# Optimization experiments

Measured on AMD Instinct MI355X. Metric: run time of the kernel, lower is better.

## Reference

```python
import jax, jax.numpy as jnp
import numpy as np

EPS = 0.5
MIN_SAMPLES = 5


def setup_inputs() -> dict:
    key = jax.random.key(0)
    X = jax.random.uniform(key, (12288, 8), dtype=jnp.float32)
    return {"X": X}


def reference(X):
    """DBSCAN: eps-range queries + cluster expansion, expressed as
    eps-graph connected components over core points (same clustering
    as the serial BFS in the original module; cluster ids are assigned
    in order of each cluster's minimum core index, matching the
    ascending-scan discovery order of the original)."""
    N = X.shape[0]
    SENTINEL = jnp.int32(N)

    # pairwise squared Euclidean distances [N, N] (KDTree range query equivalent)
    sq = jnp.sum(X * X, axis=1)
    d2 = sq[:, None] + sq[None, :] - 2.0 * (X @ X.T)
    adj = d2 <= (EPS * EPS)                      # eps-neighborhood (includes self)

    density = jnp.sum(adj, axis=1)               # |query_ball_point(x_i, eps)|
    core = density >= MIN_SAMPLES                # core-point mask

    # core-core edges: BFS expansion only propagates through cores
    core_adj = adj & core[None, :] & core[:, None]

    idx = jnp.arange(N, dtype=jnp.int32)
    init = jnp.where(core, idx, SENTINEL)        # each core starts as its own root

    def prop(lbl):
        # min label over core neighbors (min-plus propagation = connected components)
        nb_min = jnp.min(jnp.where(core_adj, lbl[None, :], SENTINEL), axis=1)
        return jnp.minimum(lbl, nb_min)

    def cond(state):
        cur, prev = state
        return jnp.any(cur != prev)

    def body(state):
        cur, _ = state
        return prop(cur), cur

    lbl, _ = jax.lax.while_loop(cond, body, (prop(init), init))

    # border points: non-core points within eps of a core join that core's cluster
    core_nb = jnp.min(jnp.where(adj & core[None, :], lbl[None, :], SENTINEL), axis=1)
    root = jnp.where(core, lbl, core_nb)         # SENTINEL -> noise

    # compact cluster ids: rank of each cluster root (min core index) ascending,
    # matching the original's sequential discovery order k = 0, 1, ...
    is_root = core & (lbl == idx)
    rank = jnp.cumsum(is_root.astype(jnp.int32)) - 1   # rank[i] valid where is_root[i]
    labels = jnp.where(root < SENTINEL,
                       rank[jnp.clip(root, 0, N - 1)],
                       jnp.int32(-1))
    return labels
```

## Files before the change

kernel.cpp:

```cpp
#include <hip/hip_runtime.h>

#define NPTS 12288
#define DIMS 8
#define EPS2 0.25f
#define MINS 5
#define NIB1 (NPTS / 256)
#define NW   (NPTS / 32)
#define SENT NPTS
#define RMAX 512
#define W    (RMAX / 32)
#define BIGL 0x3fffffff
#define FT   128
#define FB   256
#define FBGRID 256

#define ATHR 256
#define AROWS 2
#define ATI  (ATHR * AROWS)
#define ANIB (NPTS / ATI)
#define ANJB 48
#define AJC  (NPTS / ANJB)
#define AWCH (AJC / 32)

typedef float v2f __attribute__((ext_vector_type(2)));

__device__ __forceinline__ float dot8(const v2f* xi, const float4& a, const float4& b) {
  v2f y0 = {a.x, a.y}, y1 = {a.z, a.w}, y2 = {b.x, b.y}, y3 = {b.z, b.w};
  v2f d = xi[0] * y0;
  d = __builtin_elementwise_fma(xi[1], y1, d);
  d = __builtin_elementwise_fma(xi[2], y2, d);
  d = __builtin_elementwise_fma(xi[3], y3, d);
  return d.x + d.y;
}


__global__ __launch_bounds__(ATHR) void k_adj(const float* __restrict__ X,
                                              unsigned int* __restrict__ adj,
                                              int* __restrict__ density) {
  __shared__ float4 xs[AJC][2];
  __shared__ float sqs[AJC];
  int t = threadIdx.x;
  int j0 = blockIdx.y * AJC;
  {
    int j = j0 + t;
    float4 a = ((const float4*)X)[j * 2];
    float4 b = ((const float4*)X)[j * 2 + 1];
    xs[t][0] = a; xs[t][1] = b;
    float sv = 0.f;
    sv = fmaf(a.x, a.x, sv); sv = fmaf(a.y, a.y, sv); sv = fmaf(a.z, a.z, sv); sv = fmaf(a.w, a.w, sv);
    sv = fmaf(b.x, b.x, sv); sv = fmaf(b.y, b.y, sv); sv = fmaf(b.z, b.z, sv); sv = fmaf(b.w, b.w, sv);
    sqs[t] = sv;
  }
  int i0 = blockIdx.x * ATI + t, i1 = i0 + ATHR;
  v2f xi0[4], xi1[4];
  {
    float4 a0 = ((const float4*)X)[i0 * 2], b0v = ((const float4*)X)[i0 * 2 + 1];
    float4 a1 = ((const float4*)X)[i1 * 2], b1v = ((const float4*)X)[i1 * 2 + 1];
    xi0[0] = (v2f){a0.x, a0.y}; xi0[1] = (v2f){a0.z, a0.w};
    xi0[2] = (v2f){b0v.x, b0v.y}; xi0[3] = (v2f){b0v.z, b0v.w};
    xi1[0] = (v2f){a1.x, a1.y}; xi1[1] = (v2f){a1.z, a1.w};
    xi1[2] = (v2f){b1v.x, b1v.y}; xi1[3] = (v2f){b1v.z, b1v.w};
  }
  float sq0 = 0.f, sq1 = 0.f;
#pragma unroll
  for (int q = 0; q < 4; q++) {
    v2f p0 = xi0[q] * xi0[q], p1 = xi1[q] * xi1[q];
    sq0 += p0.x + p0.y; sq1 += p1.x + p1.y;
  }
  __syncthreads();
  unsigned int acc0[AWCH], acc1[AWCH];
#pragma unroll
  for (int w = 0; w < AWCH; w++) {
    unsigned int b0 = 0u, b1 = 0u;
#pragma unroll 4
    for (int bit = 0; bit < 32; bit++) {
      int jj = (w << 5) + bit;
      float4 xa = xs[jj][0], xb = xs[jj][1];
      float sj = sqs[jj];
      unsigned int m = 1u << bit;
      float d20 = (sq0 + sj) - 2.0f * dot8(xi0, xa, xb);
      float d21 = (sq1 + sj) - 2.0f * dot8(xi1, xa, xb);
      if (d20 <= EPS2) b0 |= m;
      if (d21 <= EPS2) b1 |= m;
    }
    acc0[w] = b0; acc1[w] = b1;
  }
  uint4* dst0 = (uint4*)(adj + (size_t)i0 * NW + blockIdx.y * AWCH);
  uint4* dst1 = (uint4*)(adj + (size_t)i1 * NW + blockIdx.y * AWCH);
  dst0[0] = make_uint4(acc0[0], acc0[1], acc0[2], acc0[3]);
  dst0[1] = make_uint4(acc0[4], acc0[5], acc0[6], acc0[7]);
  dst1[0] = make_uint4(acc1[0], acc1[1], acc1[2], acc1[3]);
  dst1[1] = make_uint4(acc1[4], acc1[5], acc1[6], acc1[7]);
  int pc0 = 0, pc1 = 0;
#pragma unroll
  for (int w = 0; w < AWCH; w++) { pc0 += __popc(acc0[w]); pc1 += __popc(acc1[w]); }
  atomicAdd(&density[i0], pc0);
  atomicAdd(&density[i1], pc1);
}

__global__ __launch_bounds__(256) void k_core(const int* __restrict__ density,
                                              unsigned long long* __restrict__ corebm,
                                              unsigned int* __restrict__ bm) {
  int t = threadIdx.x;
  if (blockIdx.x == 0) {
#pragma unroll
    for (int q = 0; q < RMAX * W / 256; q++) bm[t + q * 256] = 0u;
  }
  int i = blockIdx.x * 256 + t;
  unsigned long long m = __ballot(density[i] >= MINS);
  if ((t & 63) == 0) corebm[i >> 6] = m;
}

__global__ __launch_bounds__(256) void k_hookbm(const unsigned int* __restrict__ adj,
                                                const unsigned int* __restrict__ cb32,
                                                int* __restrict__ hook) {
  __shared__ unsigned int cb[NW];
  int t = threadIdx.x;
  for (int w = t; w < NW; w += 256) cb[w] = cb32[w];
  __syncthreads();
  int i = blockIdx.x * 256 + t;
  const unsigned int* row = adj + (size_t)i * NW;
  int wi = i >> 5;
  int m = i;
  for (int w = 0; w <= wi; w++) {
    unsigned int x = row[w] & cb[w];
    if (w == wi) x &= (1u << (i & 31)) - 1;
    if (x) { m = (w << 5) + __ffs(x) - 1; break; }
  }
  hook[i] = m;
}

__global__ __launch_bounds__(1024) void k_rid(const int* __restrict__ density,
                                              const int* __restrict__ hook,
                                              int* __restrict__ Rptr,
                                              int* __restrict__ labL,
                                              int* __restrict__ bcount) {
  __shared__ unsigned short ridS[NPTS];
  __shared__ int wsum[16];
  int t = threadIdx.x;
  int lane = t & 63, wid = t >> 6;
  const int SEG = NPTS / 1024;
  int base = t * SEG;
  int flags = 0;
  int s = 0;
#pragma unroll
  for (int k = 0; k < SEG; k++) {
    int i = base + k;
    int f = (density[i] >= MINS && hook[i] == i) ? 1 : 0;
    flags |= f << k;
    s += f;
  }
  int segsum = s;
#pragma unroll
  for (int off = 1; off < 64; off <<= 1) {
    int n = __shfl_up(s, off, 64);
    if (lane >= off) s += n;
  }
  if (lane == 63) wsum[wid] = s;
  __syncthreads();
  int woff = 0;
  for (int w = 0; w < wid; w++) woff += wsum[w];
  int run = woff + s - segsum;
#pragma unroll
  for (int k = 0; k < SEG; k++) {
    ridS[base + k] = (unsigned short)run;
    run += (flags >> k) & 1;
  }
  if (t == 1023) *Rptr = run;
  if (t == 0) *bcount = 0;
  __syncthreads();
  for (int k = 0; k < SEG; k++) {
    int i = base + k;
    int lab = -1;
    if (density[i] >= MINS) {
      int v = i, h = hook[v];
      while (h != v) { v = h; h = hook[v]; }
      lab = min((int)ridS[v], RMAX - 1);
    }
    labL[i] = lab;
  }
}

__global__ __launch_bounds__(FB) void k_fillbm(const unsigned int* __restrict__ adj,
                                               const unsigned int* __restrict__ cb32,
                                               const int* __restrict__ labL,
                                               unsigned int* __restrict__ bm) {
  __shared__ unsigned int bmL[RMAX * W];
  __shared__ unsigned short labS[NPTS];
  __shared__ unsigned int cb[NW];
  int t = threadIdx.x;
  for (int q = t; q < RMAX * W; q += FB) bmL[q] = 0u;
  for (int q = t; q < NPTS; q += FB) labS[q] = (unsigned short)(labL[q] + 1);
  for (int w = t; w < NW; w += FB) cb[w] = cb32[w];
  __syncthreads();
  int lane = t & 63, wv = t >> 6;
  int gw = blockIdx.x * 4 + wv;
  for (int i = gw; i < NPTS; i += 4 * FBGRID) {
    int a0 = (int)labS[i] - 1;
    if (a0 < 0) continue;
    const unsigned int* row = adj + (size_t)i * NW;
    int wi = i >> 5;
    for (int w = wi + lane; w < NW; w += 64) {
      unsigned int x = row[w] & cb[w];
      if (w == wi) x &= (0xFFFFFFFEu << (i & 31));
      while (x) {
        int b = __ffs(x) - 1; x &= x - 1;
        int lj = (int)labS[(w << 5) + b] - 1;
        if (lj != a0) {
          atomicOr(&bmL[a0 * W + (lj >> 5)], 1u << (lj & 31));
          atomicOr(&bmL[lj * W + (a0 >> 5)], 1u << (a0 & 31));
        }
      }
    }
  }
  __syncthreads();
  for (int q = t; q < RMAX * W; q += FB) {
    unsigned int v = bmL[q];
    if (v) atomicOr(&bm[q], v);
  }
}

__global__ __launch_bounds__(RMAX) void k_cc(const unsigned int* __restrict__ bm,
                                             const int* __restrict__ Rptr,
                                             int* __restrict__ clab) {
  __shared__ int lbl[RMAX];
  __shared__ int mn[RMAX];
  __shared__ int chg, cmp;
  int a = threadIdx.x;
  int R = *Rptr; if (R > RMAX) R = RMAX;
  lbl[a] = a;
  __syncthreads();
  while (true) {
    int m = lbl[a];
    if (a < R) {
      const unsigned int* row = bm + a * W;
#pragma unroll
      for (int w = 0; w < W; w++) {
        unsigned int bits = row[w];
        while (bits) {
          int b = __ffs(bits) - 1;
          bits &= bits - 1;
          m = min(m, lbl[(w << 5) + b]);
        }
      }
    }
    mn[a] = m;
    if (a == 0) chg = 0;
    __syncthreads();
    int l = lbl[a];
    if (m < l) { atomicMin(&lbl[l], m); atomicMin(&lbl[a], m); chg = 1; }
    __syncthreads();
    while (true) {
      if (a == 0) cmp = 0;
      __syncthreads();
      int nl = lbl[lbl[a]];
      __syncthreads();
      if (nl < lbl[a]) { lbl[a] = nl; cmp = 1; }
      __syncthreads();
      if (!cmp) break;
    }
    if (!chg) break;
    __syncthreads();
  }
  int flag = (a < R && lbl[a] == a) ? 1 : 0;
  mn[a] = flag;
  __syncthreads();
  for (int off = 1; off < RMAX; off <<= 1) {
    int v = mn[a];
    int add = (a >= off) ? mn[a - off] : 0;
    __syncthreads();
    mn[a] = v + add;
    __syncthreads();
  }
  clab[a] = mn[lbl[a]] - 1;
}

__global__ __launch_bounds__(256) void k_labels(const int* __restrict__ labL,
                                                const int* __restrict__ clab,
                                                int* __restrict__ labArr,
                                                int* __restrict__ blist,
                                                int* __restrict__ bcount,
                                                float* __restrict__ out) {
  int i = blockIdx.x * blockDim.x + threadIdx.x;
  if (i >= NPTS) return;
  int a = labL[i];
  if (a >= 0) {
    int lab = clab[a];
    labArr[i] = lab;
    out[i] = (float)lab;
  } else {
    labArr[i] = BIGL;
    out[i] = -1.0f;
    int pos = atomicAdd(bcount, 1);
    blist[pos] = i;
  }
}

__global__ __launch_bounds__(FT) void k_border(const unsigned int* __restrict__ adj,
                                               const unsigned int* __restrict__ cb32,
                                               const int* __restrict__ labArr,
                                               const int* __restrict__ blist,
                                               const int* __restrict__ bcount,
                                               float* __restrict__ out) {
  __shared__ unsigned int cb[NW];
  __shared__ int wm[FT / 64];
  int t = threadIdx.x;
  for (int w = t; w < NW; w += FT) cb[w] = cb32[w];
  __syncthreads();
  int count = *bcount;
  for (int k = blockIdx.x; k < count; k += gridDim.x) {
    int p = blist[k];
    const unsigned int* row = adj + (size_t)p * NW;
    int m = BIGL;
    for (int w = t; w < NW; w += FT) {
      unsigned int x = row[w] & cb[w];
      while (x) {
        int b = __ffs(x) - 1; x &= x - 1;
        m = min(m, labArr[(w << 5) + b]);
      }
    }
#pragma unroll
    for (int off = 32; off >= 1; off >>= 1) m = min(m, __shfl_xor(m, off, 64));
    if ((t & 63) == 0) wm[t >> 6] = m;
    __syncthreads();
    if (t == 0) {
      int mm = min(wm[0], wm[1]);
      out[p] = (mm < BIGL) ? (float)mm : -1.0f;
    }
    __syncthreads();
  }
}


extern "C" void kernel_launch(void* const* d_in, const int* in_sizes, int n_in,
                              void* d_out, int out_size, void* d_ws, size_t ws_size,
                              hipStream_t stream) {
  const float* X = (const float*)d_in[0];
  float* out = (float*)d_out;

  char* ws = (char*)d_ws;
  unsigned int* adj = (unsigned int*)ws;
  size_t off = (size_t)NPTS * NW * 4;
  int* density = (int*)(ws + off);           off += 4 * NPTS;
  int* hook    = (int*)(ws + off);           off += 4 * NPTS;
  int* labL    = (int*)(ws + off);           off += 4 * NPTS;
  int* labArr  = (int*)(ws + off);           off += 4 * NPTS;
  int* blist   = (int*)(ws + off);           off += 4 * NPTS;
  unsigned long long* corebm = (unsigned long long*)(ws + off); off += 2048;
  unsigned int* bm  = (unsigned int*)(ws + off); off += 4 * RMAX * W;
  int* clab    = (int*)(ws + off);           off += 4 * RMAX;
  int* Rptr    = (int*)(ws + off);
  int* bcount  = Rptr + 1;

  hipMemsetAsync(density, 0, 4 * NPTS, stream);

  dim3 gridA(ANIB, ANJB);

  k_adj<<<gridA, ATHR, 0, stream>>>(X, adj, density);
  k_core<<<NIB1, 256, 0, stream>>>(density, corebm, bm);
  k_hookbm<<<NIB1, 256, 0, stream>>>(adj, (const unsigned int*)corebm, hook);
  k_rid<<<1, 1024, 0, stream>>>(density, hook, Rptr, labL, bcount);
  k_fillbm<<<FBGRID, FB, 0, stream>>>(adj, (const unsigned int*)corebm, labL, bm);
  k_cc<<<1, RMAX, 0, stream>>>(bm, Rptr, clab);
  k_labels<<<NIB1, 256, 0, stream>>>(labL, clab, labArr, blist, bcount, out);
  k_border<<<256, FT, 0, stream>>>(adj, (const unsigned int*)corebm, labArr, blist, bcount, out);
}
```

Before: 229.1 us.

## Restructure adjacency kernel to build bitmask words via wavefront ballots

The adjacency kernel now assigns j-points to lanes and loops over a shared-memory tile of i-points. Each comparison becomes a wavefront ballot that directly yields a 64-bit mask, replacing per-thread serial bit assembly. Masks are transposed through double-buffered shared memory so each row is written with coalesced uint4 stores. Density is accumulated per j-column, which relies on the adjacency being symmetric; this adds a block barrier per 64-row group and extra select instructions per comparison.

```diff
diff --git a/kernel.cpp b/kernel.cpp
--- a/kernel.cpp
+++ b/kernel.cpp
@@ -14,88 +14,99 @@
 #define FB   256
 #define FBGRID 256
 
-#define ATHR 256
-#define AROWS 2
-#define ATI  (ATHR * AROWS)
-#define ANIB (NPTS / ATI)
-#define ANJB 48
-#define AJC  (NPTS / ANJB)
-#define AWCH (AJC / 32)
+#define AIT 256
+#define AJT 512
 
 typedef float v2f __attribute__((ext_vector_type(2)));
 
-__device__ __forceinline__ float dot8(const v2f* xi, const float4& a, const float4& b) {
-  v2f y0 = {a.x, a.y}, y1 = {a.z, a.w}, y2 = {b.x, b.y}, y3 = {b.z, b.w};
-  v2f d = xi[0] * y0;
-  d = __builtin_elementwise_fma(xi[1], y1, d);
-  d = __builtin_elementwise_fma(xi[2], y2, d);
-  d = __builtin_elementwise_fma(xi[3], y3, d);
-  return d.x + d.y;
-}
-
-
-__global__ __launch_bounds__(ATHR) void k_adj(const float* __restrict__ X,
-                                              unsigned int* __restrict__ adj,
-                                              int* __restrict__ density) {
-  __shared__ float4 xs[AJC][2];
-  __shared__ float sqs[AJC];
-  int t = threadIdx.x;
-  int j0 = blockIdx.y * AJC;
+__device__ __forceinline__ float sq8(const float4& a, const float4& b) {
+  float sv = 0.f;
+  sv = fmaf(a.x, a.x, sv); sv = fmaf(a.y, a.y, sv);
+  sv = fmaf(a.z, a.z, sv); sv = fmaf(a.w, a.w, sv);
+  sv = fmaf(b.x, b.x, sv); sv = fmaf(b.y, b.y, sv);
+  sv = fmaf(b.z, b.z, sv); sv = fmaf(b.w, b.w, sv);
+  return sv;
+}
+
+
+__global__ __launch_bounds__(256) void k_adj(const float* __restrict__ X,
+                                             unsigned int* __restrict__ adj,
+                                             int* __restrict__ density) {
+  __shared__ float4 xsh[AIT][2];
+  __shared__ float sqsh[AIT];
+  __shared__ uint4 tr[2][4][64];
+  const int t = threadIdx.x;
+  const int w = t >> 6, lane = t & 63;
+  const int i0 = blockIdx.x * AIT;
+  const int j0 = blockIdx.y * AJT;
+
   {
-    int j = j0 + t;
-    float4 a = ((const float4*)X)[j * 2];
-    float4 b = ((const float4*)X)[j * 2 + 1];
-    xs[t][0] = a; xs[t][1] = b;
-    float sv = 0.f;
-    sv = fmaf(a.x, a.x, sv); sv = fmaf(a.y, a.y, sv); sv = fmaf(a.z, a.z, sv); sv = fmaf(a.w, a.w, sv);
-    sv = fmaf(b.x, b.x, sv); sv = fmaf(b.y, b.y, sv); sv = fmaf(b.z, b.z, sv); sv = fmaf(b.w, b.w, sv);
-    sqs[t] = sv;
-  }
-  int i0 = blockIdx.x * ATI + t, i1 = i0 + ATHR;
-  v2f xi0[4], xi1[4];
+    float4 a = ((const float4*)X)[(size_t)(i0 + t) * 2];
+    float4 b = ((const float4*)X)[(size_t)(i0 + t) * 2 + 1];
+    xsh[t][0] = a; xsh[t][1] = b;
+    sqsh[t] = sq8(a, b);
+  }
+
+  const int ja = j0 + w * 128 + lane;
+  const int jb = ja + 64;
+  v2f xja[4], xjb[4];
+  float sqja, sqjb;
   {
-    float4 a0 = ((const float4*)X)[i0 * 2], b0v = ((const float4*)X)[i0 * 2 + 1];
-    float4 a1 = ((const float4*)X)[i1 * 2], b1v = ((const float4*)X)[i1 * 2 + 1];
-    xi0[0] = (v2f){a0.x, a0.y}; xi0[1] = (v2f){a0.z, a0.w};
-    xi0[2] = (v2f){b0v.x, b0v.y}; xi0[3] = (v2f){b0v.z, b0v.w};
-    xi1[0] = (v2f){a1.x, a1.y}; xi1[1] = (v2f){a1.z, a1.w};
-    xi1[2] = (v2f){b1v.x, b1v.y}; xi1[3] = (v2f){b1v.z, b1v.w};
-  }
-  float sq0 = 0.f, sq1 = 0.f;
-#pragma unroll
-  for (int q = 0; q < 4; q++) {
-    v2f p0 = xi0[q] * xi0[q], p1 = xi1[q] * xi1[q];
-    sq0 += p0.x + p0.y; sq1 += p1.x + p1.y;
-  }
-  __syncthreads();
-  unsigned int acc0[AWCH], acc1[AWCH];
-#pragma unroll
-  for (int w = 0; w < AWCH; w++) {
-    unsigned int b0 = 0u, b1 = 0u;
-#pragma unroll 4
-    for (int bit = 0; bit < 32; bit++) {
-      int jj = (w << 5) + bit;
-      float4 xa = xs[jj][0], xb = xs[jj][1];
-      float sj = sqs[jj];
-      unsigned int m = 1u << bit;
-      float d20 = (sq0 + sj) - 2.0f * dot8(xi0, xa, xb);
-      float d21 = (sq1 + sj) - 2.0f * dot8(xi1, xa, xb);
-      if (d20 <= EPS2) b0 |= m;
-      if (d21 <= EPS2) b1 |= m;
-    }
-    acc0[w] = b0; acc1[w] = b1;
-  }
-  uint4* dst0 = (uint4*)(adj + (size_t)i0 * NW + blockIdx.y * AWCH);
-  uint4* dst1 = (uint4*)(adj + (size_t)i1 * NW + blockIdx.y * AWCH);
-  dst0[0] = make_uint4(acc0[0], acc0[1], acc0[2], acc0[3]);
-  dst0[1] = make_uint4(acc0[4], acc0[5], acc0[6], acc0[7]);
-  dst1[0] = make_uint4(acc1[0], acc1[1], acc1[2], acc1[3]);
-  dst1[1] = make_uint4(acc1[4], acc1[5], acc1[6], acc1[7]);
-  int pc0 = 0, pc1 = 0;
-#pragma unroll
-  for (int w = 0; w < AWCH; w++) { pc0 += __popc(acc0[w]); pc1 += __popc(acc1[w]); }
-  atomicAdd(&density[i0], pc0);
-  atomicAdd(&density[i1], pc1);
+    float4 a = ((const float4*)X)[(size_t)ja * 2];
+    float4 b = ((const float4*)X)[(size_t)ja * 2 + 1];
+    xja[0] = (v2f){a.x, a.y}; xja[1] = (v2f){a.z, a.w};
+    xja[2] = (v2f){b.x, b.y}; xja[3] = (v2f){b.z, b.w};
+    sqja = sq8(a, b);
+  }
+  {
+    float4 a = ((const float4*)X)[(size_t)jb * 2];
+    float4 b = ((const float4*)X)[(size_t)jb * 2 + 1];
+    xjb[0] = (v2f){a.x, a.y}; xjb[1] = (v2f){a.z, a.w};
+    xjb[2] = (v2f){b.x, b.y}; xjb[3] = (v2f){b.z, b.w};
+    sqjb = sq8(a, b);
+  }
+
+  int dj0 = 0, dj1 = 0;
+  __syncthreads();
+
+  for (int g = 0; g < AIT / 64; ++g) {
+    unsigned int r0 = 0, r1 = 0, r2 = 0, r3 = 0;
+#pragma unroll 16
+    for (int ii = 0; ii < 64; ++ii) {
+      int i = (g << 6) + ii;
+      float4 A = xsh[i][0], B = xsh[i][1];
+      float si = sqsh[i];
+      v2f d0 = (v2f){A.x, A.y} * xja[0];
+      d0 = __builtin_elementwise_fma((v2f){A.z, A.w}, xja[1], d0);
+      d0 = __builtin_elementwise_fma((v2f){B.x, B.y}, xja[2], d0);
+      d0 = __builtin_elementwise_fma((v2f){B.z, B.w}, xja[3], d0);
+      v2f d1 = (v2f){A.x, A.y} * xjb[0];
+      d1 = __builtin_elementwise_fma((v2f){A.z, A.w}, xjb[1], d1);
+      d1 = __builtin_elementwise_fma((v2f){B.x, B.y}, xjb[2], d1);
+      d1 = __builtin_elementwise_fma((v2f){B.z, B.w}, xjb[3], d1);
+      float d20 = (si + sqja) - 2.0f * (d0.x + d0.y);
+      float d21 = (si + sqjb) - 2.0f * (d1.x + d1.y);
+      bool c0 = d20 <= EPS2;
+      bool c1 = d21 <= EPS2;
+      unsigned long long m0 = __ballot(c0);
+      unsigned long long m1 = __ballot(c1);
+      dj0 += c0; dj1 += c1;
+      unsigned int m0lo = (unsigned int)m0, m0hi = (unsigned int)(m0 >> 32);
+      unsigned int m1lo = (unsigned int)m1, m1hi = (unsigned int)(m1 >> 32);
+      bool mine = (lane == ii);
+      r0 = mine ? m0lo : r0;
+      r1 = mine ? m0hi : r1;
+      r2 = mine ? m1lo : r2;
+      r3 = mine ? m1hi : r3;
+    }
+    tr[g & 1][w][lane] = make_uint4(r0, r1, r2, r3);
+    __syncthreads();
+    uint4 v = tr[g & 1][t & 3][t >> 2];
+    *(uint4*)(adj + (size_t)(i0 + (g << 6) + (t >> 2)) * NW
+              + blockIdx.y * 16 + (t & 3) * 4) = v;
+  }
+  atomicAdd(&density[ja], dj0);
+  atomicAdd(&density[jb], dj1);
 }
 
 __global__ __launch_bounds__(256) void k_core(const int* __restrict__ density,
@@ -354,9 +365,9 @@
 
   hipMemsetAsync(density, 0, 4 * NPTS, stream);
 
-  dim3 gridA(ANIB, ANJB);
-
-  k_adj<<<gridA, ATHR, 0, stream>>>(X, adj, density);
+  dim3 gridA(NPTS / AIT, NPTS / AJT);
+
+  k_adj<<<gridA, 256, 0, stream>>>(X, adj, density);
   k_core<<<NIB1, 256, 0, stream>>>(density, corebm, bm);
   k_hookbm<<<NIB1, 256, 0, stream>>>(adj, (const unsigned int*)corebm, hook);
   k_rid<<<1, 1024, 0, stream>>>(density, hook, Rptr, labL, bcount);
```

Result: slower. 240.4 us (+4.9%).

## Exploit adjacency symmetry: compute upper-triangular tiles and mirror via bit transpose

Applied to the files above, without the earlier changes.

The pairwise-distance bitmask kernel now launches only the upper-triangular tile blocks (600 instead of 24x48) and writes each tile both directly and transposed. The transpose uses a 32x32 bit transpose via warp shuffles plus a shared-memory staging buffer. Diagonal tiles use masked partial writes so that no entry is written twice. This roughly halves the distance arithmetic, but adds shuffles, shared-memory traffic, a barrier and an extra set of scattered global stores and atomics per block.

```diff
diff --git a/kernel.cpp b/kernel.cpp
--- a/kernel.cpp
+++ b/kernel.cpp
@@ -17,10 +17,9 @@
 #define ATHR 256
 #define AROWS 2
 #define ATI  (ATHR * AROWS)
-#define ANIB (NPTS / ATI)
-#define ANJB 48
-#define AJC  (NPTS / ANJB)
+#define AJC  256
 #define AWCH (AJC / 32)
+#define NBLK 600
 
 typedef float v2f __attribute__((ext_vector_type(2)));
 
@@ -33,16 +32,38 @@
   return d.x + d.y;
 }
 
+__device__ __forceinline__ unsigned int tr32(unsigned int x, int lane31) {
+  const unsigned int M[5] = {0x0000FFFFu, 0x00FF00FFu, 0x0F0F0F0Fu,
+                             0x33333333u, 0x55555555u};
+  const int S[5] = {16, 8, 4, 2, 1};
+#pragma unroll
+  for (int k = 0; k < 5; ++k) {
+    int s = S[k];
+    unsigned int m = M[k];
+    unsigned int p = __shfl_xor(x, s, 32);
+    x = (lane31 & s) ? ((x & ~m) | ((p >> s) & m))
+                     : ((x & m) | ((p & m) << s));
+  }
+  return x;
+}
+
 
 __global__ __launch_bounds__(ATHR) void k_adj(const float* __restrict__ X,
                                               unsigned int* __restrict__ adj,
                                               int* __restrict__ density) {
   __shared__ float4 xs[AJC][2];
   __shared__ float sqs[AJC];
-  int t = threadIdx.x;
-  int j0 = blockIdx.y * AJC;
+  __shared__ unsigned int mir[256 * 17];
+  int t = threadIdx.x;
+
+  int B = blockIdx.x;
+  int bx = 0;
+  while ((bx + 1) * (49 - (bx + 1)) <= B) bx++;
+  int by = 2 * bx + (B - bx * (49 - bx));
+  bool full = (by >= 2 * bx + 2);
+
   {
-    int j = j0 + t;
+    int j = by * AJC + t;
     float4 a = ((const float4*)X)[j * 2];
     float4 b = ((const float4*)X)[j * 2 + 1];
     xs[t][0] = a; xs[t][1] = b;
@@ -51,7 +72,7 @@
     sv = fmaf(b.x, b.x, sv); sv = fmaf(b.y, b.y, sv); sv = fmaf(b.z, b.z, sv); sv = fmaf(b.w, b.w, sv);
     sqs[t] = sv;
   }
-  int i0 = blockIdx.x * ATI + t, i1 = i0 + ATHR;
+  int i0 = bx * ATI + t, i1 = i0 + ATHR;
   v2f xi0[4], xi1[4];
   {
     float4 a0 = ((const float4*)X)[i0 * 2], b0v = ((const float4*)X)[i0 * 2 + 1];
@@ -85,17 +106,61 @@
     }
     acc0[w] = b0; acc1[w] = b1;
   }
-  uint4* dst0 = (uint4*)(adj + (size_t)i0 * NW + blockIdx.y * AWCH);
-  uint4* dst1 = (uint4*)(adj + (size_t)i1 * NW + blockIdx.y * AWCH);
-  dst0[0] = make_uint4(acc0[0], acc0[1], acc0[2], acc0[3]);
-  dst0[1] = make_uint4(acc0[4], acc0[5], acc0[6], acc0[7]);
-  dst1[0] = make_uint4(acc1[0], acc1[1], acc1[2], acc1[3]);
-  dst1[1] = make_uint4(acc1[4], acc1[5], acc1[6], acc1[7]);
-  int pc0 = 0, pc1 = 0;
-#pragma unroll
-  for (int w = 0; w < AWCH; w++) { pc0 += __popc(acc0[w]); pc1 += __popc(acc1[w]); }
-  atomicAdd(&density[i0], pc0);
-  atomicAdd(&density[i1], pc1);
+
+  if (full) {
+    uint4* dst0 = (uint4*)(adj + (size_t)i0 * NW + by * AWCH);
+    uint4* dst1 = (uint4*)(adj + (size_t)i1 * NW + by * AWCH);
+    dst0[0] = make_uint4(acc0[0], acc0[1], acc0[2], acc0[3]);
+    dst0[1] = make_uint4(acc0[4], acc0[5], acc0[6], acc0[7]);
+    dst1[0] = make_uint4(acc1[0], acc1[1], acc1[2], acc1[3]);
+    dst1[1] = make_uint4(acc1[4], acc1[5], acc1[6], acc1[7]);
+    int pc0 = 0, pc1 = 0;
+#pragma unroll
+    for (int w = 0; w < AWCH; w++) { pc0 += __popc(acc0[w]); pc1 += __popc(acc1[w]); }
+    atomicAdd(&density[i0], pc0);
+    atomicAdd(&density[i1], pc1);
+  } else {
+    int lw0 = min(max((i0 >> 5) - 8 * by, 0), 8);
+    int lw1 = min(max((i1 >> 5) - 8 * by, 0), 8);
+    unsigned int* dst0 = adj + (size_t)i0 * NW + by * AWCH;
+    unsigned int* dst1 = adj + (size_t)i1 * NW + by * AWCH;
+    int pc0 = 0, pc1 = 0;
+    for (int wl = lw0; wl < 8; wl++) { dst0[wl] = acc0[wl]; pc0 += __popc(acc0[wl]); }
+    for (int wl = lw1; wl < 8; wl++) { dst1[wl] = acc1[wl]; pc1 += __popc(acc1[wl]); }
+    if (lw0 < 8) atomicAdd(&density[i0], pc0);
+    if (lw1 < 8) atomicAdd(&density[i1], pc1);
+  }
+
+  const int lane31 = t & 31;
+  const int hi = (t >> 5) & 1;
+  const int wv = t >> 6;
+#pragma unroll
+  for (int wl = 0; wl < AWCH; ++wl) {
+    unsigned int x0 = tr32(acc0[wl], lane31);
+    unsigned int x1 = tr32(acc1[wl], lane31);
+    int rr = (wl << 5) + lane31;
+    mir[rr * 17 + (wv << 1) + hi] = x0;
+    mir[rr * 17 + 8 + (wv << 1) + hi] = x1;
+  }
+  __syncthreads();
+  int rglob = by * 256 + t;
+  const unsigned int* mrow = &mir[t * 17];
+  unsigned int* dstm = adj + (size_t)rglob * NW + bx * 16;
+  if (full) {
+    ((uint4*)dstm)[0] = make_uint4(mrow[0], mrow[1], mrow[2], mrow[3]);
+    ((uint4*)dstm)[1] = make_uint4(mrow[4], mrow[5], mrow[6], mrow[7]);
+    ((uint4*)dstm)[2] = make_uint4(mrow[8], mrow[9], mrow[10], mrow[11]);
+    ((uint4*)dstm)[3] = make_uint4(mrow[12], mrow[13], mrow[14], mrow[15]);
+    int pc = 0;
+#pragma unroll
+    for (int q = 0; q < 16; q++) pc += __popc(mrow[q]);
+    atomicAdd(&density[rglob], pc);
+  } else {
+    int nv = min(max((rglob >> 5) - 16 * bx, 0), 16);
+    int pc = 0;
+    for (int q = 0; q < nv; q++) { dstm[q] = mrow[q]; pc += __popc(mrow[q]); }
+    if (nv > 0) atomicAdd(&density[rglob], pc);
+  }
 }
 
 __global__ __launch_bounds__(256) void k_core(const int* __restrict__ density,
@@ -354,9 +419,7 @@
 
   hipMemsetAsync(density, 0, 4 * NPTS, stream);
 
-  dim3 gridA(ANIB, ANJB);
-
-  k_adj<<<gridA, ATHR, 0, stream>>>(X, adj, density);
+  k_adj<<<NBLK, ATHR, 0, stream>>>(X, adj, density);
   k_core<<<NIB1, 256, 0, stream>>>(density, corebm, bm);
   k_hookbm<<<NIB1, 256, 0, stream>>>(adj, (const unsigned int*)corebm, hook);
   k_rid<<<1, 1024, 0, stream>>>(density, hook, Rptr, labL, bcount);
```

New measurement: 217.1 us. 1.05x faster.
